# Performance work log

Hardware: AMD Instinct MI355X
Metric: run time of the kernel (lower is better)

Reference implementation:

```python
import jax, jax.numpy as jnp
import numpy as np

EPS = 1e-4      # forward() default eps
SEP = 0.01      # interval-separation slack used in original
NORM_EPS = 1e-12  # torch F.normalize eps


def _intervals(vp, vd):
    """Moller-style interval endpoints. vp, vd: [F, F, 3].
    Replicates the 3-way branch (vd0*vd1>0 / vd0*vd2>0 / else) with where-selects.
    Returns (min, max) of the two intersection parameters, shape [F, F]."""
    vp0, vp1, vp2 = vp[..., 0], vp[..., 1], vp[..., 2]
    vd0, vd1, vd2 = vd[..., 0], vd[..., 1], vd[..., 2]
    c1 = vd0 * vd1 > 0
    c2 = (~c1) & (vd0 * vd2 > 0)
    # permuted (a0, a1, a2) / (d0, d1, d2) per branch:
    #   c1 -> (p2,p0,p1)/(d2,d0,d1); c2 -> (p1,p0,p2)/(d1,d0,d2); else identity
    a0 = jnp.where(c1, vp2, jnp.where(c2, vp1, vp0))
    a1 = jnp.where(c1, vp0, jnp.where(c2, vp0, vp1))
    a2 = jnp.where(c1, vp1, vp2)
    d0 = jnp.where(c1, vd2, jnp.where(c2, vd1, vd0))
    d1 = jnp.where(c1, vd0, jnp.where(c2, vd0, vd1))
    d2 = jnp.where(c1, vd1, vd2)
    i0 = a0 + (a1 - a0) * (d0 / (d0 - d1 + EPS))
    i1 = a0 + (a2 - a0) * (d0 / (d0 - d2 + EPS))
    return jnp.minimum(i0, i1), jnp.maximum(i0, i1)


def setup_inputs() -> dict:
    key = jax.random.key(0)
    k1, k2, k3 = jax.random.split(key, 3)
    V, F = 1280, 2500
    vertices = jax.random.normal(k1, (1, V, 3), dtype=jnp.float32)
    faces_normals = jax.random.normal(k2, (1, F, 3), dtype=jnp.float32)
    faces = jax.random.randint(k3, (F, 3), 0, V, dtype=jnp.int64)
    return {"vertices": vertices, "faces_normals": faces_normals, "faces": faces}


def reference(vertices, faces_normals, faces):
    # vertices: [1, V, 3], faces_normals: [1, F, 3], faces: [F, 3] int
    verts = vertices[0]           # [V, 3]
    n = faces_normals[0]          # [F, 3]
    v0, v1, v2 = faces[:, 0], faces[:, 1], faces[:, 2]
    U = jnp.stack([verts[v0], verts[v1], verts[v2]], axis=0)  # [3, F, 3]
    # plane offset for face i: d1[i] = -p0_i . n_i
    d1 = -jnp.einsum('fd,fd->f', verts[v0], n)                # [F]
    # DU[i, j, k] = (vertex k of face j) . n_i + d1[i]
    DU = jnp.einsum('kjd,id->ijk', U, n) + d1[:, None, None]  # [F, F, 3]
    keep = ~(jnp.all(DU + EPS > 0, axis=-1) | jnp.all(DU - EPS < 0, axis=-1))
    keep = keep & keep.T                                      # [F, F]
    # projection direction D[i, j] = normalize(n_i x n_j)
    Dvec = jnp.cross(n[:, None, :], n[None, :, :])            # [F, F, 3]
    Dvec = Dvec / jnp.maximum(
        jnp.linalg.norm(Dvec, axis=-1, keepdims=True), NORM_EPS)
    # Up[i, j, k] = D[i, j] . (vertex k of face j)
    Up = jnp.einsum('ijd,kjd->ijk', Dvec, U)                  # [F, F, 3]
    lo0, hi0 = _intervals(Up, DU)
    lo1, hi1 = _intervals(-jnp.swapaxes(Up, 0, 1), jnp.swapaxes(DU, 0, 1))
    sep = (hi0 <= lo1 + SEP) | (hi1 <= lo0 + SEP)             # intervals disjoint
    F_ = n.shape[0]
    upper = jnp.triu(jnp.ones((F_, F_), dtype=bool), k=1)
    kill = sep & keep & upper   # original only tests i < j, applies symmetrically
    keep = keep & ~(kill | kill.T)
    row = jnp.sum(keep, axis=1).astype(vertices.dtype)        # [F]
    loss = (jnp.sum(vertices[:, v0, 0] * row)
            + 2.0 * jnp.sum(vertices[:, v2, 0] * row)) / 3.0
    return loss
```

## Files before the change

### kernel.cpp

```cpp
#include <hip/hip_runtime.h>

typedef float f32x4 __attribute__((ext_vector_type(4)));

#define VL_EPS  1e-4f
#define VL_SEP  0.01f
#define VL_NEPS 1e-12f

__device__ __forceinline__ void vl_intervals(float p0, float p1, float p2,
                                             float d0, float d1, float d2,
                                             float& lo, float& hi) {
  bool c1 = (d0 * d1) > 0.0f;
  bool c2 = (!c1) && ((d0 * d2) > 0.0f);
  float a0, a1, a2, e0, e1, e2;
  if (c1)      { a0 = p2; a1 = p0; a2 = p1; e0 = d2; e1 = d0; e2 = d1; }
  else if (c2) { a0 = p1; a1 = p0; a2 = p2; e0 = d1; e1 = d0; e2 = d2; }
  else         { a0 = p0; a1 = p1; a2 = p2; e0 = d0; e1 = d1; e2 = d2; }
  float i0 = a0 + (a1 - a0) * (e0 / (e0 - e1 + VL_EPS));
  float i1 = a0 + (a2 - a0) * (e0 / (e0 - e2 + VL_EPS));
  lo = fminf(i0, i1);
  hi = fmaxf(i0, i1);
}

__device__ __forceinline__ int vl_tail(
    float iu0x, float iu0y, float iu0z,
    float iu1x, float iu1y, float iu1z,
    float iu2x, float iu2y, float iu2z,
    float nxi, float nyi, float nzi,
    float ju0x, float ju0y, float ju0z,
    float ju1x, float ju1y, float ju1z,
    float ju2x, float ju2y, float ju2z,
    float nxj, float nyj, float nzj,
    float dij0, float dij1, float dij2,
    float dji0, float dji1, float dji2,
    int gi, int gj) {
  const float cx = nyi * nzj - nzi * nyj;
  const float cy = nzi * nxj - nxi * nzj;
  const float cz = nxi * nyj - nyi * nxj;
  const float nrm = sqrtf(cx * cx + cy * cy + cz * cz);
  const float inv = 1.0f / fmaxf(nrm, VL_NEPS);
  const float dx = cx * inv, dy = cy * inv, dz = cz * inv;

  const float pa0 = dx * ju0x + dy * ju0y + dz * ju0z;
  const float pa1 = dx * ju1x + dy * ju1y + dz * ju1z;
  const float pa2 = dx * ju2x + dy * ju2y + dz * ju2z;
  const float pb0 = dx * iu0x + dy * iu0y + dz * iu0z;
  const float pb1 = dx * iu1x + dy * iu1y + dz * iu1z;
  const float pb2 = dx * iu2x + dy * iu2y + dz * iu2z;

  float aLo, aHi, bLo, bHi;
  vl_intervals(pa0, pa1, pa2, dij0, dij1, dij2, aLo, aHi);
  vl_intervals(pb0, pb1, pb2, dji0, dji1, dji2, bLo, bHi);

  bool sep_;
  if (gi < gj) sep_ = (aHi <= bLo + VL_SEP) || (bHi <= aLo + VL_SEP);
  else         sep_ = false;

  return sep_ ? 0 : 1;
}

__global__ __launch_bounds__(256) void vl_pair(const float* __restrict__ verts,
                                               const float* __restrict__ fnorm,
                                               const int*   __restrict__ faces,
                                               float* __restrict__ partial,
                                               int F) {
  __shared__ float sI[13 * 64];
  __shared__ float sJ[13 * 64];
  __shared__ unsigned short qbuf[4][256];
  __shared__ int srowI[64];
  __shared__ int srowJ[64];
  __shared__ float sred[256];

  const int t    = threadIdx.x;
  const int lane = t & 63;
  const int w    = t >> 6;

  const int k = blockIdx.x;
  int by = (int)((sqrtf(8.0f * (float)k + 1.0f) - 1.0f) * 0.5f);
  while ((by + 1) * (by + 2) / 2 <= k) ++by;
  while (by * (by + 1) / 2 > k) --by;
  const int bx = k - by * (by + 1) / 2;
  const int bi = bx * 64;
  const int bj = by * 64;
  const bool dg = (bx == by);

  if (t < 128) {
    const bool isI = (t < 64);
    const int  lf  = t & 63;
    const int  f   = (isI ? bi : bj) + lf;
    float* dst = isI ? sI : sJ;
    float v[13];
#pragma unroll
    for (int c = 0; c < 13; ++c) v[c] = 0.0f;
    if (f < F) {
      const int va = faces[3 * f + 0];
      const int vb = faces[3 * f + 1];
      const int vc = faces[3 * f + 2];
      v[0] = verts[3 * va + 0]; v[1]  = verts[3 * va + 1]; v[2]  = verts[3 * va + 2];
      v[3] = verts[3 * vb + 0]; v[4]  = verts[3 * vb + 1]; v[5]  = verts[3 * vb + 2];
      v[6] = verts[3 * vc + 0]; v[7]  = verts[3 * vc + 1]; v[8]  = verts[3 * vc + 2];
      v[9] = fnorm[3 * f + 0];  v[10] = fnorm[3 * f + 1]; v[11] = fnorm[3 * f + 2];
      v[12] = -(v[0] * v[9] + v[1] * v[10] + v[2] * v[11]);
    }
#pragma unroll
    for (int c = 0; c < 13; ++c) dst[c * 64 + lf] = v[c];
  }
  if (t < 64) { srowI[t] = 0; srowJ[t] = 0; }
  __syncthreads();

  const int ii = lane;
  const float iu0x = sI[0 * 64 + ii], iu0y = sI[1 * 64 + ii], iu0z = sI[2 * 64 + ii];
  const float iu1x = sI[3 * 64 + ii], iu1y = sI[4 * 64 + ii], iu1z = sI[5 * 64 + ii];
  const float iu2x = sI[6 * 64 + ii], iu2y = sI[7 * 64 + ii], iu2z = sI[8 * 64 + ii];
  const float nxi  = sI[9 * 64 + ii], nyi  = sI[10 * 64 + ii], nzi = sI[11 * 64 + ii];
  const float d1i  = sI[12 * 64 + ii];

  unsigned short* qb = qbuf[w];
  int qtail = 0, qhead = 0;

  auto drain = [&](int nd) {
    if (lane < nd) {
      const int e  = qb[(qhead + lane) & 255];
      const int qi = e >> 6;
      const int qj = e & 63;
      const float A0x = sI[0 * 64 + qi], A0y = sI[1 * 64 + qi], A0z = sI[2 * 64 + qi];
      const float A1x = sI[3 * 64 + qi], A1y = sI[4 * 64 + qi], A1z = sI[5 * 64 + qi];
      const float A2x = sI[6 * 64 + qi], A2y = sI[7 * 64 + qi], A2z = sI[8 * 64 + qi];
      const float Anx = sI[9 * 64 + qi], Any = sI[10 * 64 + qi], Anz = sI[11 * 64 + qi];
      const float Ad  = sI[12 * 64 + qi];
      const float B0x = sJ[0 * 64 + qj], B0y = sJ[1 * 64 + qj], B0z = sJ[2 * 64 + qj];
      const float B1x = sJ[3 * 64 + qj], B1y = sJ[4 * 64 + qj], B1z = sJ[5 * 64 + qj];
      const float B2x = sJ[6 * 64 + qj], B2y = sJ[7 * 64 + qj], B2z = sJ[8 * 64 + qj];
      const float Bnx = sJ[9 * 64 + qj], Bny = sJ[10 * 64 + qj], Bnz = sJ[11 * 64 + qj];
      const float Bd  = sJ[12 * 64 + qj];
      const float dij0 = Anx * B0x + Any * B0y + Anz * B0z + Ad;
      const float dij1 = Anx * B1x + Any * B1y + Anz * B1z + Ad;
      const float dij2 = Anx * B2x + Any * B2y + Anz * B2z + Ad;
      const float dji0 = Bnx * A0x + Bny * A0y + Bnz * A0z + Bd;
      const float dji1 = Bnx * A1x + Bny * A1y + Bnz * A1z + Bd;
      const float dji2 = Bnx * A2x + Bny * A2y + Bnz * A2z + Bd;
      const int kk = vl_tail(A0x, A0y, A0z, A1x, A1y, A1z, A2x, A2y, A2z,
                             Anx, Any, Anz,
                             B0x, B0y, B0z, B1x, B1y, B1z, B2x, B2y, B2z,
                             Bnx, Bny, Bnz,
                             dij0, dij1, dij2, dji0, dji1, dji2,
                             bi + qi, bj + qj);
      if (kk) {
        atomicAdd(&srowI[qi], 1);
        if (!(dg && qi == qj))
          atomicAdd(dg ? &srowI[qj] : &srowJ[qj], 1);
      }
    }
    qhead += nd;
  };

  const unsigned long long lt = (1ULL << lane) - 1ULL;
#pragma unroll 2
  for (int s = 0; s < 4; ++s) {
    const int jj = (w << 2) + (s << 4);

    const f32x4 ju0x = *(const f32x4*)&sJ[0 * 64 + jj];
    const f32x4 ju0y = *(const f32x4*)&sJ[1 * 64 + jj];
    const f32x4 ju0z = *(const f32x4*)&sJ[2 * 64 + jj];
    const f32x4 ju1x = *(const f32x4*)&sJ[3 * 64 + jj];
    const f32x4 ju1y = *(const f32x4*)&sJ[4 * 64 + jj];
    const f32x4 ju1z = *(const f32x4*)&sJ[5 * 64 + jj];
    const f32x4 ju2x = *(const f32x4*)&sJ[6 * 64 + jj];
    const f32x4 ju2y = *(const f32x4*)&sJ[7 * 64 + jj];
    const f32x4 ju2z = *(const f32x4*)&sJ[8 * 64 + jj];
    const f32x4 nxj  = *(const f32x4*)&sJ[9 * 64 + jj];
    const f32x4 nyj  = *(const f32x4*)&sJ[10 * 64 + jj];
    const f32x4 nzj  = *(const f32x4*)&sJ[11 * 64 + jj];
    const f32x4 d1j  = *(const f32x4*)&sJ[12 * 64 + jj];

    const f32x4 dij0 = nxi * ju0x + nyi * ju0y + nzi * ju0z + d1i;
    const f32x4 dij1 = nxi * ju1x + nyi * ju1y + nzi * ju1z + d1i;
    const f32x4 dij2 = nxi * ju2x + nyi * ju2y + nzi * ju2z + d1i;
    const f32x4 dji0 = nxj * iu0x + nyj * iu0y + nzj * iu0z + d1j;
    const f32x4 dji1 = nxj * iu1x + nyj * iu1y + nzj * iu1z + d1j;
    const f32x4 dji2 = nxj * iu2x + nyj * iu2y + nzj * iu2z + d1j;

    const f32x4 mnv = __builtin_elementwise_max(
        __builtin_elementwise_min(__builtin_elementwise_min(dij0, dij1), dij2),
        __builtin_elementwise_min(__builtin_elementwise_min(dji0, dji1), dji2));
    const f32x4 mxv = __builtin_elementwise_min(
        __builtin_elementwise_max(__builtin_elementwise_max(dij0, dij1), dij2),
        __builtin_elementwise_max(__builtin_elementwise_max(dji0, dji1), dji2));

    bool sv[4];
#pragma unroll
    for (int q = 0; q < 4; ++q) {
      sv[q] = (mnv[q] + VL_EPS <= 0.0f) && (mxv[q] - VL_EPS >= 0.0f);
      if (dg) sv[q] = sv[q] && (ii <= jj + q);
    }

    const unsigned long long m0 = __ballot(sv[0]);
    const unsigned long long m1 = __ballot(sv[1]);
    if (m0 | m1) {
      const int n0 = __popcll(m0);
      if (sv[0]) qb[(qtail + __popcll(m0 & lt)) & 255] =
                     (unsigned short)((ii << 6) | jj);
      if (sv[1]) qb[(qtail + n0 + __popcll(m1 & lt)) & 255] =
                     (unsigned short)((ii << 6) | (jj + 1));
      qtail += n0 + __popcll(m1);
      while (qtail - qhead >= 64) drain(64);
    }
    const unsigned long long m2 = __ballot(sv[2]);
    const unsigned long long m3 = __ballot(sv[3]);
    if (m2 | m3) {
      const int n2 = __popcll(m2);
      if (sv[2]) qb[(qtail + __popcll(m2 & lt)) & 255] =
                     (unsigned short)((ii << 6) | (jj + 2));
      if (sv[3]) qb[(qtail + n2 + __popcll(m3 & lt)) & 255] =
                     (unsigned short)((ii << 6) | (jj + 3));
      qtail += n2 + __popcll(m3);
      while (qtail - qhead >= 64) drain(64);
    }
  }
  if (qtail > qhead) drain(qtail - qhead);

  __syncthreads();
  float val = 0.0f;
  if (t < 64) {
    val = (sI[0 * 64 + t] + 2.0f * sI[6 * 64 + t]) * (float)srowI[t];
  } else if (t < 128 && !dg) {
    const int l = t - 64;
    val = (sJ[0 * 64 + l] + 2.0f * sJ[6 * 64 + l]) * (float)srowJ[l];
  }
  sred[t] = val;
  __syncthreads();
#pragma unroll
  for (int r = 128; r > 0; r >>= 1) {
    if (t < r) sred[t] += sred[t + r];
    __syncthreads();
  }
  if (t == 0) partial[k] = sred[0];
}

__global__ __launch_bounds__(256) void vl_reduce(const float* __restrict__ partial,
                                                 int n, float* __restrict__ out) {
  __shared__ float s[256];
  const int t = threadIdx.x;
  float acc = 0.0f;
  for (int b = t; b < n; b += 256) acc += partial[b];
  s[t] = acc;
  __syncthreads();
  for (int r = 128; r > 0; r >>= 1) {
    if (t < r) s[t] += s[t + r];
    __syncthreads();
  }
  if (t == 0) out[0] = s[0] / 3.0f;
}

extern "C" void kernel_launch(void* const* d_in, const int* in_sizes, int n_in,
                              void* d_out, int out_size, void* d_ws, size_t ws_size,
                              hipStream_t stream) {
  const float* verts = (const float*)d_in[0];
  const float* fnorm = (const float*)d_in[1];
  const int*   faces = (const int*)d_in[2];
  const int F = in_sizes[1] / 3;

  float* partial = (float*)d_ws;

  const int NB = (F + 63) / 64;
  const int nblk = NB * (NB + 1) / 2;
  vl_pair<<<nblk, 256, 0, stream>>>(verts, fnorm, faces, partial, F);
  vl_reduce<<<1, 256, 0, stream>>>(partial, nblk, (float*)d_out);
}
```

Baseline: 21.97 us.

## Process two triangle tiles per 512-thread block, reusing the shared J-tile

Each block now has 8 wavefronts instead of 4 and loops over two consecutive upper-triangular 64x64 tiles. The eight waves split the 64 j-columns of a tile between them, so each wave handles half as many columns. When both tiles share the same row index, the J face data already in shared memory is reused instead of being gathered again. The aim is to halve the block count and cut the gather and launch cost per tile. In exchange, the two tiles run one after the other inside a block, with extra barriers and a larger final reduction.

```diff
diff --git a/kernel.cpp b/kernel.cpp
--- a/kernel.cpp
+++ b/kernel.cpp
@@ -58,64 +58,28 @@
   return sep_ ? 0 : 1;
 }
 
-__global__ __launch_bounds__(256) void vl_pair(const float* __restrict__ verts,
+__global__ __launch_bounds__(512) void vl_pair(const float* __restrict__ verts,
                                                const float* __restrict__ fnorm,
                                                const int*   __restrict__ faces,
                                                float* __restrict__ partial,
-                                               int F) {
+                                               int F, int NP) {
   __shared__ float sI[13 * 64];
   __shared__ float sJ[13 * 64];
-  __shared__ unsigned short qbuf[4][256];
+  __shared__ unsigned short qbuf[8][256];
   __shared__ int srowI[64];
   __shared__ int srowJ[64];
-  __shared__ float sred[256];
+  __shared__ float sred[512];
 
   const int t    = threadIdx.x;
   const int lane = t & 63;
   const int w    = t >> 6;
-
-  const int k = blockIdx.x;
-  int by = (int)((sqrtf(8.0f * (float)k + 1.0f) - 1.0f) * 0.5f);
-  while ((by + 1) * (by + 2) / 2 <= k) ++by;
-  while (by * (by + 1) / 2 > k) --by;
-  const int bx = k - by * (by + 1) / 2;
-  const int bi = bx * 64;
-  const int bj = by * 64;
-  const bool dg = (bx == by);
-
-  if (t < 128) {
-    const bool isI = (t < 64);
-    const int  lf  = t & 63;
-    const int  f   = (isI ? bi : bj) + lf;
-    float* dst = isI ? sI : sJ;
-    float v[13];
-#pragma unroll
-    for (int c = 0; c < 13; ++c) v[c] = 0.0f;
-    if (f < F) {
-      const int va = faces[3 * f + 0];
-      const int vb = faces[3 * f + 1];
-      const int vc = faces[3 * f + 2];
-      v[0] = verts[3 * va + 0]; v[1]  = verts[3 * va + 1]; v[2]  = verts[3 * va + 2];
-      v[3] = verts[3 * vb + 0]; v[4]  = verts[3 * vb + 1]; v[5]  = verts[3 * vb + 2];
-      v[6] = verts[3 * vc + 0]; v[7]  = verts[3 * vc + 1]; v[8]  = verts[3 * vc + 2];
-      v[9] = fnorm[3 * f + 0];  v[10] = fnorm[3 * f + 1]; v[11] = fnorm[3 * f + 2];
-      v[12] = -(v[0] * v[9] + v[1] * v[10] + v[2] * v[11]);
-    }
-#pragma unroll
-    for (int c = 0; c < 13; ++c) dst[c * 64 + lf] = v[c];
-  }
-  if (t < 64) { srowI[t] = 0; srowJ[t] = 0; }
-  __syncthreads();
-
-  const int ii = lane;
-  const float iu0x = sI[0 * 64 + ii], iu0y = sI[1 * 64 + ii], iu0z = sI[2 * 64 + ii];
-  const float iu1x = sI[3 * 64 + ii], iu1y = sI[4 * 64 + ii], iu1z = sI[5 * 64 + ii];
-  const float iu2x = sI[6 * 64 + ii], iu2y = sI[7 * 64 + ii], iu2z = sI[8 * 64 + ii];
-  const float nxi  = sI[9 * 64 + ii], nyi  = sI[10 * 64 + ii], nzi = sI[11 * 64 + ii];
-  const float d1i  = sI[12 * 64 + ii];
+  const unsigned long long lt = (1ULL << lane) - 1ULL;
 
   unsigned short* qb = qbuf[w];
   int qtail = 0, qhead = 0;
+
+  int bi = 0, bj = 0;
+  bool dg = false;
 
   auto drain = [&](int nd) {
     if (lane < nd) {
@@ -153,87 +117,135 @@
     qhead += nd;
   };
 
-  const unsigned long long lt = (1ULL << lane) - 1ULL;
-#pragma unroll 2
-  for (int s = 0; s < 4; ++s) {
-    const int jj = (w << 2) + (s << 4);
-
-    const f32x4 ju0x = *(const f32x4*)&sJ[0 * 64 + jj];
-    const f32x4 ju0y = *(const f32x4*)&sJ[1 * 64 + jj];
-    const f32x4 ju0z = *(const f32x4*)&sJ[2 * 64 + jj];
-    const f32x4 ju1x = *(const f32x4*)&sJ[3 * 64 + jj];
-    const f32x4 ju1y = *(const f32x4*)&sJ[4 * 64 + jj];
-    const f32x4 ju1z = *(const f32x4*)&sJ[5 * 64 + jj];
-    const f32x4 ju2x = *(const f32x4*)&sJ[6 * 64 + jj];
-    const f32x4 ju2y = *(const f32x4*)&sJ[7 * 64 + jj];
-    const f32x4 ju2z = *(const f32x4*)&sJ[8 * 64 + jj];
-    const f32x4 nxj  = *(const f32x4*)&sJ[9 * 64 + jj];
-    const f32x4 nyj  = *(const f32x4*)&sJ[10 * 64 + jj];
-    const f32x4 nzj  = *(const f32x4*)&sJ[11 * 64 + jj];
-    const f32x4 d1j  = *(const f32x4*)&sJ[12 * 64 + jj];
-
-    const f32x4 dij0 = nxi * ju0x + nyi * ju0y + nzi * ju0z + d1i;
-    const f32x4 dij1 = nxi * ju1x + nyi * ju1y + nzi * ju1z + d1i;
-    const f32x4 dij2 = nxi * ju2x + nyi * ju2y + nzi * ju2z + d1i;
-    const f32x4 dji0 = nxj * iu0x + nyj * iu0y + nzj * iu0z + d1j;
-    const f32x4 dji1 = nxj * iu1x + nyj * iu1y + nzj * iu1z + d1j;
-    const f32x4 dji2 = nxj * iu2x + nyj * iu2y + nzj * iu2z + d1j;
-
-    const f32x4 mnv = __builtin_elementwise_max(
-        __builtin_elementwise_min(__builtin_elementwise_min(dij0, dij1), dij2),
-        __builtin_elementwise_min(__builtin_elementwise_min(dji0, dji1), dji2));
-    const f32x4 mxv = __builtin_elementwise_min(
-        __builtin_elementwise_max(__builtin_elementwise_max(dij0, dij1), dij2),
-        __builtin_elementwise_max(__builtin_elementwise_max(dji0, dji1), dji2));
-
-    bool sv[4];
-#pragma unroll
-    for (int q = 0; q < 4; ++q) {
-      sv[q] = (mnv[q] + VL_EPS <= 0.0f) && (mxv[q] - VL_EPS >= 0.0f);
-      if (dg) sv[q] = sv[q] && (ii <= jj + q);
-    }
-
-    const unsigned long long m0 = __ballot(sv[0]);
-    const unsigned long long m1 = __ballot(sv[1]);
-    if (m0 | m1) {
-      const int n0 = __popcll(m0);
-      if (sv[0]) qb[(qtail + __popcll(m0 & lt)) & 255] =
-                     (unsigned short)((ii << 6) | jj);
-      if (sv[1]) qb[(qtail + n0 + __popcll(m1 & lt)) & 255] =
-                     (unsigned short)((ii << 6) | (jj + 1));
-      qtail += n0 + __popcll(m1);
-      while (qtail - qhead >= 64) drain(64);
-    }
-    const unsigned long long m2 = __ballot(sv[2]);
-    const unsigned long long m3 = __ballot(sv[3]);
-    if (m2 | m3) {
-      const int n2 = __popcll(m2);
-      if (sv[2]) qb[(qtail + __popcll(m2 & lt)) & 255] =
-                     (unsigned short)((ii << 6) | (jj + 2));
-      if (sv[3]) qb[(qtail + n2 + __popcll(m3 & lt)) & 255] =
-                     (unsigned short)((ii << 6) | (jj + 3));
-      qtail += n2 + __popcll(m3);
-      while (qtail - qhead >= 64) drain(64);
-    }
+  float lacc = 0.0f;
+  int prev_by = -1;
+
+  for (int k = 2 * blockIdx.x; k < 2 * blockIdx.x + 2 && k < NP; ++k) {
+    int by = (int)((sqrtf(8.0f * (float)k + 1.0f) - 1.0f) * 0.5f);
+    while ((by + 1) * (by + 2) / 2 <= k) ++by;
+    while (by * (by + 1) / 2 > k) --by;
+    const int bx = k - by * (by + 1) / 2;
+    bi = bx * 64;
+    bj = by * 64;
+    dg = (bx == by);
+    const bool newrow = (by != prev_by);
+    prev_by = by;
+
+    if (t < 128) {
+      const bool isI = (t < 64);
+      if (isI || newrow) {
+        const int  lf = t & 63;
+        const int  f  = (isI ? bi : bj) + lf;
+        float* dst = isI ? sI : sJ;
+        float v[13];
+#pragma unroll
+        for (int c = 0; c < 13; ++c) v[c] = 0.0f;
+        if (f < F) {
+          const int va = faces[3 * f + 0];
+          const int vb = faces[3 * f + 1];
+          const int vc = faces[3 * f + 2];
+          v[0] = verts[3 * va + 0]; v[1]  = verts[3 * va + 1]; v[2]  = verts[3 * va + 2];
+          v[3] = verts[3 * vb + 0]; v[4]  = verts[3 * vb + 1]; v[5]  = verts[3 * vb + 2];
+          v[6] = verts[3 * vc + 0]; v[7]  = verts[3 * vc + 1]; v[8]  = verts[3 * vc + 2];
+          v[9] = fnorm[3 * f + 0];  v[10] = fnorm[3 * f + 1]; v[11] = fnorm[3 * f + 2];
+          v[12] = -(v[0] * v[9] + v[1] * v[10] + v[2] * v[11]);
+        }
+#pragma unroll
+        for (int c = 0; c < 13; ++c) dst[c * 64 + lf] = v[c];
+      }
+    }
+    if (t < 64) { srowI[t] = 0; srowJ[t] = 0; }
+    __syncthreads();
+
+    const int ii = lane;
+    const float iu0x = sI[0 * 64 + ii], iu0y = sI[1 * 64 + ii], iu0z = sI[2 * 64 + ii];
+    const float iu1x = sI[3 * 64 + ii], iu1y = sI[4 * 64 + ii], iu1z = sI[5 * 64 + ii];
+    const float iu2x = sI[6 * 64 + ii], iu2y = sI[7 * 64 + ii], iu2z = sI[8 * 64 + ii];
+    const float nxi  = sI[9 * 64 + ii], nyi  = sI[10 * 64 + ii], nzi = sI[11 * 64 + ii];
+    const float d1i  = sI[12 * 64 + ii];
+
+#pragma unroll
+    for (int s = 0; s < 2; ++s) {
+      const int jj = (w << 2) + (s << 5);
+
+      const f32x4 ju0x = *(const f32x4*)&sJ[0 * 64 + jj];
+      const f32x4 ju0y = *(const f32x4*)&sJ[1 * 64 + jj];
+      const f32x4 ju0z = *(const f32x4*)&sJ[2 * 64 + jj];
+      const f32x4 ju1x = *(const f32x4*)&sJ[3 * 64 + jj];
+      const f32x4 ju1y = *(const f32x4*)&sJ[4 * 64 + jj];
+      const f32x4 ju1z = *(const f32x4*)&sJ[5 * 64 + jj];
+      const f32x4 ju2x = *(const f32x4*)&sJ[6 * 64 + jj];
+      const f32x4 ju2y = *(const f32x4*)&sJ[7 * 64 + jj];
+      const f32x4 ju2z = *(const f32x4*)&sJ[8 * 64 + jj];
+      const f32x4 nxj  = *(const f32x4*)&sJ[9 * 64 + jj];
+      const f32x4 nyj  = *(const f32x4*)&sJ[10 * 64 + jj];
+      const f32x4 nzj  = *(const f32x4*)&sJ[11 * 64 + jj];
+      const f32x4 d1j  = *(const f32x4*)&sJ[12 * 64 + jj];
+
+      const f32x4 dij0 = nxi * ju0x + nyi * ju0y + nzi * ju0z + d1i;
+      const f32x4 dij1 = nxi * ju1x + nyi * ju1y + nzi * ju1z + d1i;
+      const f32x4 dij2 = nxi * ju2x + nyi * ju2y + nzi * ju2z + d1i;
+      const f32x4 dji0 = nxj * iu0x + nyj * iu0y + nzj * iu0z + d1j;
+      const f32x4 dji1 = nxj * iu1x + nyj * iu1y + nzj * iu1z + d1j;
+      const f32x4 dji2 = nxj * iu2x + nyj * iu2y + nzj * iu2z + d1j;
+
+      const f32x4 mnv = __builtin_elementwise_max(
+          __builtin_elementwise_min(__builtin_elementwise_min(dij0, dij1), dij2),
+          __builtin_elementwise_min(__builtin_elementwise_min(dji0, dji1), dji2));
+      const f32x4 mxv = __builtin_elementwise_min(
+          __builtin_elementwise_max(__builtin_elementwise_max(dij0, dij1), dij2),
+          __builtin_elementwise_max(__builtin_elementwise_max(dji0, dji1), dji2));
+
+      bool sv[4];
+#pragma unroll
+      for (int q = 0; q < 4; ++q) {
+        sv[q] = (mnv[q] + VL_EPS <= 0.0f) && (mxv[q] - VL_EPS >= 0.0f);
+        if (dg) sv[q] = sv[q] && (ii <= jj + q);
+      }
+
+      const unsigned long long m0 = __ballot(sv[0]);
+      const unsigned long long m1 = __ballot(sv[1]);
+      if (m0 | m1) {
+        const int n0 = __popcll(m0);
+        if (sv[0]) qb[(qtail + __popcll(m0 & lt)) & 255] =
+                       (unsigned short)((ii << 6) | jj);
+        if (sv[1]) qb[(qtail + n0 + __popcll(m1 & lt)) & 255] =
+                       (unsigned short)((ii << 6) | (jj + 1));
+        qtail += n0 + __popcll(m1);
+        while (qtail - qhead >= 64) drain(64);
+      }
+      const unsigned long long m2 = __ballot(sv[2]);
+      const unsigned long long m3 = __ballot(sv[3]);
+      if (m2 | m3) {
+        const int n2 = __popcll(m2);
+        if (sv[2]) qb[(qtail + __popcll(m2 & lt)) & 255] =
+                       (unsigned short)((ii << 6) | (jj + 2));
+        if (sv[3]) qb[(qtail + n2 + __popcll(m3 & lt)) & 255] =
+                       (unsigned short)((ii << 6) | (jj + 3));
+        qtail += n2 + __popcll(m3);
+        while (qtail - qhead >= 64) drain(64);
+      }
+    }
+    if (qtail > qhead) drain(qtail - qhead);
+
+    __syncthreads();
+    if (t < 64) {
+      lacc += (sI[0 * 64 + t] + 2.0f * sI[6 * 64 + t]) * (float)srowI[t];
+    } else if (t < 128 && !dg) {
+      const int l = t - 64;
+      lacc += (sJ[0 * 64 + l] + 2.0f * sJ[6 * 64 + l]) * (float)srowJ[l];
+    }
+    __syncthreads();
   }
-  if (qtail > qhead) drain(qtail - qhead);
-
+
+  sred[t] = lacc;
   __syncthreads();
-  float val = 0.0f;
-  if (t < 64) {
-    val = (sI[0 * 64 + t] + 2.0f * sI[6 * 64 + t]) * (float)srowI[t];
-  } else if (t < 128 && !dg) {
-    const int l = t - 64;
-    val = (sJ[0 * 64 + l] + 2.0f * sJ[6 * 64 + l]) * (float)srowJ[l];
+#pragma unroll
+  for (int r = 256; r > 0; r >>= 1) {
+    if (t < r) sred[t] += sred[t + r];
+    __syncthreads();
   }
-  sred[t] = val;
-  __syncthreads();
-#pragma unroll
-  for (int r = 128; r > 0; r >>= 1) {
-    if (t < r) sred[t] += sred[t + r];
-    __syncthreads();
-  }
-  if (t == 0) partial[k] = sred[0];
+  if (t == 0) partial[blockIdx.x] = sred[0];
 }
 
 __global__ __launch_bounds__(256) void vl_reduce(const float* __restrict__ partial,
@@ -262,7 +274,8 @@
   float* partial = (float*)d_ws;
 
   const int NB = (F + 63) / 64;
-  const int nblk = NB * (NB + 1) / 2;
-  vl_pair<<<nblk, 256, 0, stream>>>(verts, fnorm, faces, partial, F);
+  const int NP = NB * (NB + 1) / 2;
+  const int nblk = (NP + 1) / 2;
+  vl_pair<<<nblk, 512, 0, stream>>>(verts, fnorm, faces, partial, F, NP);
   vl_reduce<<<1, 256, 0, stream>>>(partial, nblk, (float*)d_out);
 }
```

Measured after the change: 25.17 us. +14.5%, slower.

## Precompute per-face gathered data in a separate kernel, read from global in pair kernel

Applied to the files above, without the earlier changes.

Moves the per-face vertex gather and plane-offset computation out of each pair block into a dedicated pre-pass kernel that writes an SoA buffer to workspace. The pair kernel then reads I and J face data directly from global/cache instead of staging it in LDS, with uniform scalar-address vector loads for the J tiles. This removes redundant indirect gathers repeated across roughly 800 blocks and a block sync before compute. In exchange it adds a kernel launch and relies on cache hits for the repeated reads in the inner loop and in the drain path.

```diff
diff --git a/kernel.cpp b/kernel.cpp
--- a/kernel.cpp
+++ b/kernel.cpp
@@ -58,13 +58,33 @@
   return sep_ ? 0 : 1;
 }
 
-__global__ __launch_bounds__(256) void vl_pair(const float* __restrict__ verts,
-                                               const float* __restrict__ fnorm,
-                                               const int*   __restrict__ faces,
+__global__ __launch_bounds__(256) void vl_gather(const float* __restrict__ verts,
+                                                 const float* __restrict__ fnorm,
+                                                 const int*   __restrict__ faces,
+                                                 float* __restrict__ gat,
+                                                 int F, int Fp) {
+  const int f = blockIdx.x * 256 + threadIdx.x;
+  if (f >= Fp) return;
+  float v[13];
+#pragma unroll
+  for (int c = 0; c < 13; ++c) v[c] = 0.0f;
+  if (f < F) {
+    const int va = faces[3 * f + 0];
+    const int vb = faces[3 * f + 1];
+    const int vc = faces[3 * f + 2];
+    v[0] = verts[3 * va + 0]; v[1]  = verts[3 * va + 1]; v[2]  = verts[3 * va + 2];
+    v[3] = verts[3 * vb + 0]; v[4]  = verts[3 * vb + 1]; v[5]  = verts[3 * vb + 2];
+    v[6] = verts[3 * vc + 0]; v[7]  = verts[3 * vc + 1]; v[8]  = verts[3 * vc + 2];
+    v[9] = fnorm[3 * f + 0];  v[10] = fnorm[3 * f + 1]; v[11] = fnorm[3 * f + 2];
+    v[12] = -(v[0] * v[9] + v[1] * v[10] + v[2] * v[11]);
+  }
+#pragma unroll
+  for (int c = 0; c < 13; ++c) gat[c * Fp + f] = v[c];
+}
+
+__global__ __launch_bounds__(256) void vl_pair(const float* __restrict__ gat,
                                                float* __restrict__ partial,
-                                               int F) {
-  __shared__ float sI[13 * 64];
-  __shared__ float sJ[13 * 64];
+                                               int F, int Fp) {
   __shared__ unsigned short qbuf[4][256];
   __shared__ int srowI[64];
   __shared__ int srowJ[64];
@@ -83,36 +103,16 @@
   const int bj = by * 64;
   const bool dg = (bx == by);
 
-  if (t < 128) {
-    const bool isI = (t < 64);
-    const int  lf  = t & 63;
-    const int  f   = (isI ? bi : bj) + lf;
-    float* dst = isI ? sI : sJ;
-    float v[13];
-#pragma unroll
-    for (int c = 0; c < 13; ++c) v[c] = 0.0f;
-    if (f < F) {
-      const int va = faces[3 * f + 0];
-      const int vb = faces[3 * f + 1];
-      const int vc = faces[3 * f + 2];
-      v[0] = verts[3 * va + 0]; v[1]  = verts[3 * va + 1]; v[2]  = verts[3 * va + 2];
-      v[3] = verts[3 * vb + 0]; v[4]  = verts[3 * vb + 1]; v[5]  = verts[3 * vb + 2];
-      v[6] = verts[3 * vc + 0]; v[7]  = verts[3 * vc + 1]; v[8]  = verts[3 * vc + 2];
-      v[9] = fnorm[3 * f + 0];  v[10] = fnorm[3 * f + 1]; v[11] = fnorm[3 * f + 2];
-      v[12] = -(v[0] * v[9] + v[1] * v[10] + v[2] * v[11]);
-    }
-#pragma unroll
-    for (int c = 0; c < 13; ++c) dst[c * 64 + lf] = v[c];
-  }
   if (t < 64) { srowI[t] = 0; srowJ[t] = 0; }
   __syncthreads();
 
   const int ii = lane;
-  const float iu0x = sI[0 * 64 + ii], iu0y = sI[1 * 64 + ii], iu0z = sI[2 * 64 + ii];
-  const float iu1x = sI[3 * 64 + ii], iu1y = sI[4 * 64 + ii], iu1z = sI[5 * 64 + ii];
-  const float iu2x = sI[6 * 64 + ii], iu2y = sI[7 * 64 + ii], iu2z = sI[8 * 64 + ii];
-  const float nxi  = sI[9 * 64 + ii], nyi  = sI[10 * 64 + ii], nzi = sI[11 * 64 + ii];
-  const float d1i  = sI[12 * 64 + ii];
+  const int fi = bi + ii;
+  const float iu0x = gat[0 * Fp + fi], iu0y = gat[1 * Fp + fi], iu0z = gat[2 * Fp + fi];
+  const float iu1x = gat[3 * Fp + fi], iu1y = gat[4 * Fp + fi], iu1z = gat[5 * Fp + fi];
+  const float iu2x = gat[6 * Fp + fi], iu2y = gat[7 * Fp + fi], iu2z = gat[8 * Fp + fi];
+  const float nxi  = gat[9 * Fp + fi], nyi  = gat[10 * Fp + fi], nzi = gat[11 * Fp + fi];
+  const float d1i  = gat[12 * Fp + fi];
 
   unsigned short* qb = qbuf[w];
   int qtail = 0, qhead = 0;
@@ -120,18 +120,18 @@
   auto drain = [&](int nd) {
     if (lane < nd) {
       const int e  = qb[(qhead + lane) & 255];
-      const int qi = e >> 6;
-      const int qj = e & 63;
-      const float A0x = sI[0 * 64 + qi], A0y = sI[1 * 64 + qi], A0z = sI[2 * 64 + qi];
-      const float A1x = sI[3 * 64 + qi], A1y = sI[4 * 64 + qi], A1z = sI[5 * 64 + qi];
-      const float A2x = sI[6 * 64 + qi], A2y = sI[7 * 64 + qi], A2z = sI[8 * 64 + qi];
-      const float Anx = sI[9 * 64 + qi], Any = sI[10 * 64 + qi], Anz = sI[11 * 64 + qi];
-      const float Ad  = sI[12 * 64 + qi];
-      const float B0x = sJ[0 * 64 + qj], B0y = sJ[1 * 64 + qj], B0z = sJ[2 * 64 + qj];
-      const float B1x = sJ[3 * 64 + qj], B1y = sJ[4 * 64 + qj], B1z = sJ[5 * 64 + qj];
-      const float B2x = sJ[6 * 64 + qj], B2y = sJ[7 * 64 + qj], B2z = sJ[8 * 64 + qj];
-      const float Bnx = sJ[9 * 64 + qj], Bny = sJ[10 * 64 + qj], Bnz = sJ[11 * 64 + qj];
-      const float Bd  = sJ[12 * 64 + qj];
+      const int qi = bi + (e >> 6);
+      const int qj = bj + (e & 63);
+      const float A0x = gat[0 * Fp + qi], A0y = gat[1 * Fp + qi], A0z = gat[2 * Fp + qi];
+      const float A1x = gat[3 * Fp + qi], A1y = gat[4 * Fp + qi], A1z = gat[5 * Fp + qi];
+      const float A2x = gat[6 * Fp + qi], A2y = gat[7 * Fp + qi], A2z = gat[8 * Fp + qi];
+      const float Anx = gat[9 * Fp + qi], Any = gat[10 * Fp + qi], Anz = gat[11 * Fp + qi];
+      const float Ad  = gat[12 * Fp + qi];
+      const float B0x = gat[0 * Fp + qj], B0y = gat[1 * Fp + qj], B0z = gat[2 * Fp + qj];
+      const float B1x = gat[3 * Fp + qj], B1y = gat[4 * Fp + qj], B1z = gat[5 * Fp + qj];
+      const float B2x = gat[6 * Fp + qj], B2y = gat[7 * Fp + qj], B2z = gat[8 * Fp + qj];
+      const float Bnx = gat[9 * Fp + qj], Bny = gat[10 * Fp + qj], Bnz = gat[11 * Fp + qj];
+      const float Bd  = gat[12 * Fp + qj];
       const float dij0 = Anx * B0x + Any * B0y + Anz * B0z + Ad;
       const float dij1 = Anx * B1x + Any * B1y + Anz * B1z + Ad;
       const float dij2 = Anx * B2x + Any * B2y + Anz * B2z + Ad;
@@ -143,11 +143,12 @@
                              B0x, B0y, B0z, B1x, B1y, B1z, B2x, B2y, B2z,
                              Bnx, Bny, Bnz,
                              dij0, dij1, dij2, dji0, dji1, dji2,
-                             bi + qi, bj + qj);
+                             qi, qj);
       if (kk) {
-        atomicAdd(&srowI[qi], 1);
-        if (!(dg && qi == qj))
-          atomicAdd(dg ? &srowI[qj] : &srowJ[qj], 1);
+        const int li = qi - bi, lj = qj - bj;
+        atomicAdd(&srowI[li], 1);
+        if (!(dg && li == lj))
+          atomicAdd(dg ? &srowI[lj] : &srowJ[lj], 1);
       }
     }
     qhead += nd;
@@ -157,20 +158,21 @@
 #pragma unroll 2
   for (int s = 0; s < 4; ++s) {
     const int jj = (w << 2) + (s << 4);
-
-    const f32x4 ju0x = *(const f32x4*)&sJ[0 * 64 + jj];
-    const f32x4 ju0y = *(const f32x4*)&sJ[1 * 64 + jj];
-    const f32x4 ju0z = *(const f32x4*)&sJ[2 * 64 + jj];
-    const f32x4 ju1x = *(const f32x4*)&sJ[3 * 64 + jj];
-    const f32x4 ju1y = *(const f32x4*)&sJ[4 * 64 + jj];
-    const f32x4 ju1z = *(const f32x4*)&sJ[5 * 64 + jj];
-    const f32x4 ju2x = *(const f32x4*)&sJ[6 * 64 + jj];
-    const f32x4 ju2y = *(const f32x4*)&sJ[7 * 64 + jj];
-    const f32x4 ju2z = *(const f32x4*)&sJ[8 * 64 + jj];
-    const f32x4 nxj  = *(const f32x4*)&sJ[9 * 64 + jj];
-    const f32x4 nyj  = *(const f32x4*)&sJ[10 * 64 + jj];
-    const f32x4 nzj  = *(const f32x4*)&sJ[11 * 64 + jj];
-    const f32x4 d1j  = *(const f32x4*)&sJ[12 * 64 + jj];
+    const int jb = __builtin_amdgcn_readfirstlane(bj + jj);
+
+    const f32x4 ju0x = *(const f32x4*)(gat + 0 * Fp + jb);
+    const f32x4 ju0y = *(const f32x4*)(gat + 1 * Fp + jb);
+    const f32x4 ju0z = *(const f32x4*)(gat + 2 * Fp + jb);
+    const f32x4 ju1x = *(const f32x4*)(gat + 3 * Fp + jb);
+    const f32x4 ju1y = *(const f32x4*)(gat + 4 * Fp + jb);
+    const f32x4 ju1z = *(const f32x4*)(gat + 5 * Fp + jb);
+    const f32x4 ju2x = *(const f32x4*)(gat + 6 * Fp + jb);
+    const f32x4 ju2y = *(const f32x4*)(gat + 7 * Fp + jb);
+    const f32x4 ju2z = *(const f32x4*)(gat + 8 * Fp + jb);
+    const f32x4 nxj  = *(const f32x4*)(gat + 9 * Fp + jb);
+    const f32x4 nyj  = *(const f32x4*)(gat + 10 * Fp + jb);
+    const f32x4 nzj  = *(const f32x4*)(gat + 11 * Fp + jb);
+    const f32x4 d1j  = *(const f32x4*)(gat + 12 * Fp + jb);
 
     const f32x4 dij0 = nxi * ju0x + nyi * ju0y + nzi * ju0z + d1i;
     const f32x4 dij1 = nxi * ju1x + nyi * ju1y + nzi * ju1z + d1i;
@@ -221,10 +223,10 @@
   __syncthreads();
   float val = 0.0f;
   if (t < 64) {
-    val = (sI[0 * 64 + t] + 2.0f * sI[6 * 64 + t]) * (float)srowI[t];
+    val = (gat[0 * Fp + bi + t] + 2.0f * gat[6 * Fp + bi + t]) * (float)srowI[t];
   } else if (t < 128 && !dg) {
     const int l = t - 64;
-    val = (sJ[0 * 64 + l] + 2.0f * sJ[6 * 64 + l]) * (float)srowJ[l];
+    val = (gat[0 * Fp + bj + l] + 2.0f * gat[6 * Fp + bj + l]) * (float)srowJ[l];
   }
   sred[t] = val;
   __syncthreads();
@@ -259,10 +261,13 @@
   const int*   faces = (const int*)d_in[2];
   const int F = in_sizes[1] / 3;
 
-  float* partial = (float*)d_ws;
-
   const int NB = (F + 63) / 64;
+  const int Fp = NB * 64;
+  float* gat     = (float*)d_ws;
+  float* partial = gat + 13 * Fp;
+
   const int nblk = NB * (NB + 1) / 2;
-  vl_pair<<<nblk, 256, 0, stream>>>(verts, fnorm, faces, partial, F);
+  vl_gather<<<(Fp + 255) / 256, 256, 0, stream>>>(verts, fnorm, faces, gat, F, Fp);
+  vl_pair<<<nblk, 256, 0, stream>>>(gat, partial, F, Fp);
   vl_reduce<<<1, 256, 0, stream>>>(partial, nblk, (float*)d_out);
 }
```

Result: slower. 30.48 us (+38.7%).
